# Optimization experiments

Hardware: AMD Instinct MI355X
Metric: run time of the kernel (lower is better)

Reference implementation:

```python
import jax, jax.numpy as jnp
import numpy as np

DIM = 256
HEADS = 8
HEAD_DIM = DIM // HEADS
SCALE = HEAD_DIM ** -0.5
SR = 2
EPS_MAP = 1e-6
EPS_LN = 1e-5


def token2map(x, loc, h, w):
    # x: [B,N,C] tokens, loc: [B,N,2] in [0,1] -> dense [B,h,w,C] via scatter-add mean.
    # kernel_size=1 in the original forward, so reconstruct_feature is a no-op.
    B, N, C = x.shape
    loc = jnp.clip(loc, 0.0, 1.0) * jnp.array([w - 1, h - 1], dtype=loc.dtype)
    loc = jnp.round(loc).astype(jnp.int32)
    idx = loc[..., 0] + loc[..., 1] * w + (jnp.arange(B, dtype=jnp.int32) * (h * w))[:, None]
    src = jnp.concatenate([x, jnp.ones((B, N, 1), x.dtype)], axis=-1).reshape(B * N, C + 1)
    out = jax.ops.segment_sum(src, idx.reshape(-1), num_segments=B * h * w)
    out = out.reshape(B, h, w, C + 1)
    feat, mask = out[..., :C], out[..., C:]
    feat = feat / (mask + EPS_MAP)
    mask = (mask > 0).astype(feat.dtype)
    return feat * mask  # [B,h,w,C]


def layernorm(x, g, b):
    mu = jnp.mean(x, axis=-1, keepdims=True)
    var = jnp.mean(jnp.square(x - mu), axis=-1, keepdims=True)
    return (x - mu) * jax.lax.rsqrt(var + EPS_LN) * g + b


def setup_inputs() -> dict:
    key = jax.random.key(0)
    ks = jax.random.split(key, 12)
    B, N, C = 4, 4096, DIM
    inp = {
        "x": jax.random.normal(ks[0], (B, N, C), jnp.float32),
        "x_source": jax.random.normal(ks[1], (B, N, C), jnp.float32),
        "loc_source": jax.random.uniform(ks[2], (B, N, 2), jnp.float32),
        "conf_source": jax.random.normal(ks[3], (B, N, 1), jnp.float32),
        "Wq": jax.random.normal(ks[4], (C, C), jnp.float32) * 0.02,
        "Wk": jax.random.normal(ks[5], (C, C), jnp.float32) * 0.02,
        "Wv": jax.random.normal(ks[6], (C, C), jnp.float32) * 0.02,
        "Wsr": jax.random.normal(ks[7], (C, C), jnp.float32) * 0.02,
        "b_sr": jnp.zeros((C,), jnp.float32),
        "ln_g": jnp.ones((C,), jnp.float32),
        "ln_b": jnp.zeros((C,), jnp.float32),
        "Wp": jax.random.normal(ks[8], (C, C), jnp.float32) * 0.02,
        "bp": jnp.zeros((C,), jnp.float32),
        "H": 64,
        "W": 64,
    }
    return inp


def reference(x, x_source, loc_source, conf_source, Wq, Wk, Wv, Wsr, b_sr, ln_g, ln_b, Wp, bp, H, W):
    B, N, C = x.shape
    h, w = H // SR, W // SR
    # queries
    q = (x @ Wq.T).reshape(B, N, HEADS, HEAD_DIM).transpose(0, 2, 1, 3)  # [B,h,N,d]
    # rasterize source tokens, 1x1 conv (sr) + LayerNorm
    xs = token2map(x_source, loc_source, h, w).reshape(B, h * w, C)
    xs = xs @ Wsr.T + b_sr
    xs = layernorm(xs, ln_g, ln_b)  # [B,Ns,C]
    Ns = h * w
    k = (xs @ Wk.T).reshape(B, Ns, HEADS, HEAD_DIM).transpose(0, 2, 1, 3)
    v = (xs @ Wv.T).reshape(B, Ns, HEADS, HEAD_DIM).transpose(0, 2, 1, 3)
    # rasterized confidence as additive bias
    conf = token2map(conf_source, loc_source, h, w).reshape(B, Ns)  # [B,Ns]
    attn = jnp.einsum("bhnd,bhmd->bhnm", q, k) * SCALE + conf[:, None, None, :]
    attn = jax.nn.softmax(attn, axis=-1)
    out = jnp.einsum("bhnm,bhmd->bhnd", attn, v).transpose(0, 2, 1, 3).reshape(B, N, C)
    return out @ Wp.T + bp
```

## Files before the change

### kernel.cpp

```cpp
#include <hip/hip_runtime.h>
#include <math.h>

#define DIMC   256
#define NQ     4096
#define BATCH  4
#define NS     1024
#define WG     32
#define HG     32
#define NHEADS 8
#define HDIM   32
#define TILEK  128
#define KSTRIDE 40
#define VSTRIDE 136
#define WSTRIDE 264
#define BUCKCAP 64
#define GCELLS 4
#define SCALE_ATTN 0.17677669529663687
#define LOG2E 1.4426950408889634
#define SCALE2F ((float)(SCALE_ATTN * LOG2E))

extern "C" __device__ float __ocml_native_exp2_f32(float);
#if __has_builtin(__builtin_amdgcn_exp2f)
#define EXP2(x) __builtin_amdgcn_exp2f(x)
#else
#define EXP2(x) __ocml_native_exp2_f32(x)
#endif

typedef _Float16 f16;
typedef __attribute__((ext_vector_type(8))) __bf16    bf16x8;
typedef __attribute__((ext_vector_type(8))) _Float16  f16x8;
typedef __attribute__((ext_vector_type(4))) _Float16  f16x4;
typedef __attribute__((ext_vector_type(4))) float     f32x4;

#define MFMA16B(A, B, C)  __builtin_amdgcn_mfma_f32_16x16x32_bf16((A), (B), (C), 0, 0, 0)
#define MFMA16F(A, B, C)  __builtin_amdgcn_mfma_f32_16x16x32_f16((A), (B), (C), 0, 0, 0)
#define MFMA16K16(A, B, C) __builtin_amdgcn_mfma_f32_16x16x16f16((A), (B), (C), 0, 0, 0)

static __device__ __forceinline__ unsigned short bf16_hi(float v) {
    return __builtin_bit_cast(unsigned short, (__bf16)v);
}

__global__ __launch_bounds__(256) void prep_kernel(
    const float* __restrict__ Wsr, const float* __restrict__ Wq,
    const float* __restrict__ Wk, const float* __restrict__ Wv,
    const float* __restrict__ Wp,
    unsigned short* __restrict__ wsrh, unsigned short* __restrict__ wsrl,
    f16* __restrict__ wq16, f16* __restrict__ wkv, f16* __restrict__ wp16,
    int* __restrict__ cursor)
{
    int m = blockIdx.y;
    if (m == 5) {
        int i = blockIdx.x * 256 + threadIdx.x;
        if (i < BATCH * NS) cursor[i] = 0;
        return;
    }
    int i = (blockIdx.x * 256 + threadIdx.x) * 4;
    if (m == 0) {
        float4 v = *(const float4*)(Wsr + i);
        float vv[4] = {v.x, v.y, v.z, v.w};
        ushort4 h, l;
        unsigned short* hp = &h.x; unsigned short* lp = &l.x;
        #pragma unroll
        for (int j = 0; j < 4; j++) {
            __bf16 hb = (__bf16)vv[j];
            hp[j] = __builtin_bit_cast(unsigned short, hb);
            lp[j] = bf16_hi(vv[j] - (float)hb);
        }
        *(ushort4*)(wsrh + i) = h;
        *(ushort4*)(wsrl + i) = l;
    } else {
        const float* W = (m == 1) ? Wq : (m == 2) ? Wk : (m == 3) ? Wv : Wp;
        f16* O = (m == 1) ? wq16 : (m == 2) ? wkv
               : (m == 3) ? (wkv + DIMC * DIMC) : wp16;
        float4 v = *(const float4*)(W + i);
        f16x4 h = {(f16)v.x, (f16)v.y, (f16)v.z, (f16)v.w};
        *(f16x4*)(O + i) = h;
    }
}

__global__ __launch_bounds__(256) void build_kernel(
    const float* __restrict__ loc, int* __restrict__ cursor,
    int* __restrict__ bucket)
{
    int token = blockIdx.x * 256 + threadIdx.x;
    int b = token >> 12;
    float lx = loc[token * 2 + 0];
    float ly = loc[token * 2 + 1];
    lx = fminf(fmaxf(lx, 0.f), 1.f) * (float)(WG - 1);
    ly = fminf(fmaxf(ly, 0.f), 1.f) * (float)(HG - 1);
    int ix = (int)rintf(lx);
    int iy = (int)rintf(ly);
    int cell = b * NS + iy * WG + ix;
    int slot = atomicAdd(&cursor[cell], 1);
    if (slot < BUCKCAP) bucket[cell * BUCKCAP + slot] = token;
}

__global__ __launch_bounds__(256) void gather_kernel(
    const float* __restrict__ xsrc, const float* __restrict__ csrc,
    const int* __restrict__ cursor, const int* __restrict__ bucket,
    float* __restrict__ feat, float* __restrict__ cnt, float* __restrict__ confsum)
{
    __shared__ int bks[GCELLS][BUCKCAP];
    __shared__ int ns[GCELLS];
    int cell0 = blockIdx.x * GCELLS;
    int tid = threadIdx.x;
    int jw = tid >> 6, slot = tid & 63;
    int cj = cell0 + jw;
    int rawn = cursor[cj];
    if (slot == 0) ns[jw] = min(rawn, BUCKCAP);
    bks[jw][slot] = bucket[(size_t)cj * BUCKCAP + slot];
    __syncthreads();
    int nw = ns[jw];
    float cv = (slot < nw) ? csrc[bks[jw][slot]] : 0.f;
    #pragma unroll
    for (int off = 1; off < 64; off <<= 1) cv += __shfl_xor(cv, off);
    if (slot == 0) { confsum[cj] = cv; cnt[cj] = (float)rawn; }
    int c = tid;
    for (int j = 0; j < GCELLS; j++) {
        int n = ns[j];
        float s0 = 0.f, s1 = 0.f, s2 = 0.f, s3 = 0.f;
        int i = 0;
        for (; i + 4 <= n; i += 4) {
            s0 += xsrc[(size_t)bks[j][i]     * DIMC + c];
            s1 += xsrc[(size_t)bks[j][i + 1] * DIMC + c];
            s2 += xsrc[(size_t)bks[j][i + 2] * DIMC + c];
            s3 += xsrc[(size_t)bks[j][i + 3] * DIMC + c];
        }
        for (; i < n; i++)
            s0 += xsrc[(size_t)bks[j][i] * DIMC + c];
        feat[(size_t)(cell0 + j) * DIMC + c] = (s0 + s1) + (s2 + s3);
    }
}

__global__ __launch_bounds__(256) void gemm_sr_kernel(
    const float* __restrict__ A, const float* __restrict__ cnt,
    const float* __restrict__ confsum,
    const unsigned short* __restrict__ Whi, const unsigned short* __restrict__ Wlo,
    const float* __restrict__ bias, float* __restrict__ outF,
    float2* __restrict__ stats, float* __restrict__ conf2)
{
    int r0 = blockIdx.x * 16;
    int wave = threadIdx.x >> 6;
    int lane = threadIdx.x & 63;
    int s = lane & 15, g = lane >> 4;
    int arow = r0 + s;
    int cb = wave * 64;
    const float* ap = A + (size_t)arow * DIMC + 8 * g;
    float cv = cnt[arow];
    float invr = (cv > 0.f) ? 1.f / (cv + 1e-6f) : 0.f;

    f32x4 acc[4];
    #pragma unroll
    for (int cf = 0; cf < 4; cf++) {
        float bv = bias[cb + cf * 16 + s];
        acc[cf] = (f32x4){bv, bv, bv, bv};
    }

    #pragma unroll
    for (int kk = 0; kk < 8; kk++) {
        float4 a0 = *(const float4*)(ap + kk * 32);
        float4 a1 = *(const float4*)(ap + kk * 32 + 4);
        float av[8] = {a0.x, a0.y, a0.z, a0.w, a1.x, a1.y, a1.z, a1.w};
        bf16x8 ah, al;
        #pragma unroll
        for (int j = 0; j < 8; j++) {
            float v = av[j] * invr;
            __bf16 hb = (__bf16)v;
            ah[j] = hb;
            al[j] = (__bf16)(v - (float)hb);
        }
        #pragma unroll
        for (int cf = 0; cf < 4; cf++) {
            size_t woff = (size_t)(cb + cf * 16 + s) * DIMC + kk * 32 + 8 * g;
            bf16x8 bh = *(const bf16x8*)(Whi + woff);
            bf16x8 bl = *(const bf16x8*)(Wlo + woff);
            acc[cf] = MFMA16B(ah, bh, acc[cf]);
            acc[cf] = MFMA16B(al, bh, acc[cf]);
            acc[cf] = MFMA16B(ah, bl, acc[cf]);
        }
    }

    int rbase = r0 + 4 * g;
    #pragma unroll
    for (int cf = 0; cf < 4; cf++) {
        int c = cb + cf * 16 + s;
        #pragma unroll
        for (int r = 0; r < 4; r++)
            outF[(size_t)(rbase + r) * DIMC + c] = acc[cf][r];
    }
    float psum[4], psq[4];
    #pragma unroll
    for (int r = 0; r < 4; r++) {
        psum[r] = 0.f; psq[r] = 0.f;
        #pragma unroll
        for (int cf = 0; cf < 4; cf++) {
            float v = acc[cf][r];
            psum[r] += v; psq[r] += v * v;
        }
    }
    #pragma unroll
    for (int off = 1; off < 16; off <<= 1)
        #pragma unroll
        for (int r = 0; r < 4; r++) {
            psum[r] += __shfl_xor(psum[r], off);
            psq[r]  += __shfl_xor(psq[r], off);
        }
    __shared__ float ssum[4][16], ssq[4][16];
    if (s == 0)
        #pragma unroll
        for (int r = 0; r < 4; r++) {
            ssum[wave][4 * g + r] = psum[r];
            ssq[wave][4 * g + r]  = psq[r];
        }
    __syncthreads();
    if (threadIdx.x < 16) {
        int rr = threadIdx.x;
        float su = ssum[0][rr] + ssum[1][rr] + ssum[2][rr] + ssum[3][rr];
        float sq = ssq[0][rr] + ssq[1][rr] + ssq[2][rr] + ssq[3][rr];
        float mu  = su * (1.f / DIMC);
        float var = sq * (1.f / DIMC) - mu * mu;
        stats[r0 + rr] = make_float2(mu, rsqrtf(var + 1e-5f));
        float cv2 = cnt[r0 + rr];
        float iv2 = (cv2 > 0.f) ? 1.f / (cv2 + 1e-6f) : 0.f;
        conf2[r0 + rr] = confsum[r0 + rr] * iv2 * (float)LOG2E;
    }
}

__global__ __launch_bounds__(256) void gemm_kv_kernel(
    const float* __restrict__ xs, const float2* __restrict__ stats,
    const float* __restrict__ lng, const float* __restrict__ lnb,
    const f16* __restrict__ wkv, f16* __restrict__ k16, f16* __restrict__ vt16)
{
    int r0 = blockIdx.x * 16;
    int cb0 = blockIdx.y * 128;
    int wave = threadIdx.x >> 6;
    int lane = threadIdx.x & 63;
    int s = lane & 15, g = lane >> 4;
    int arow = r0 + s;
    int cb = cb0 + wave * 32;
    float2 st = stats[arow];
    const float* ap = xs + (size_t)arow * DIMC + 8 * g;

    f32x4 acc[2];
    acc[0] = (f32x4){0.f, 0.f, 0.f, 0.f};
    acc[1] = (f32x4){0.f, 0.f, 0.f, 0.f};

    #pragma unroll
    for (int kk = 0; kk < 8; kk++) {
        float4 a0 = *(const float4*)(ap + kk * 32);
        float4 a1 = *(const float4*)(ap + kk * 32 + 4);
        float4 g0 = *(const float4*)(lng + kk * 32 + 8 * g);
        float4 g1 = *(const float4*)(lng + kk * 32 + 8 * g + 4);
        float4 b0 = *(const float4*)(lnb + kk * 32 + 8 * g);
        float4 b1 = *(const float4*)(lnb + kk * 32 + 8 * g + 4);
        float av[8] = {a0.x, a0.y, a0.z, a0.w, a1.x, a1.y, a1.z, a1.w};
        float gv[8] = {g0.x, g0.y, g0.z, g0.w, g1.x, g1.y, g1.z, g1.w};
        float bv[8] = {b0.x, b0.y, b0.z, b0.w, b1.x, b1.y, b1.z, b1.w};
        f16x8 a;
        #pragma unroll
        for (int j = 0; j < 8; j++)
            a[j] = (f16)(((av[j] - st.x) * st.y) * gv[j] + bv[j]);
        #pragma unroll
        for (int cf = 0; cf < 2; cf++) {
            f16x8 bfrag = *(const f16x8*)(wkv + (size_t)(cb + cf * 16 + s) * DIMC
                                              + kk * 32 + 8 * g);
            acc[cf] = MFMA16F(a, bfrag, acc[cf]);
        }
    }

    int rbase = r0 + 4 * g;
    if (cb0 < 256) {
        #pragma unroll
        for (int cf = 0; cf < 2; cf++) {
            int c = cb + cf * 16 + s;
            #pragma unroll
            for (int r = 0; r < 4; r++)
                k16[(size_t)(rbase + r) * DIMC + c] = (f16)acc[cf][r];
        }
    } else {
        int b = rbase >> 10;
        int key0 = rbase & 1023;
        #pragma unroll
        for (int cf = 0; cf < 2; cf++) {
            int cc = cb + cf * 16 + s - 256;
            f16x4 h;
            #pragma unroll
            for (int r = 0; r < 4; r++) h[r] = (f16)acc[cf][r];
            size_t off = ((size_t)(b * DIMC + cc)) * NS + key0;
            *(f16x4*)(vt16 + off) = h;
        }
    }
}

template <bool A16, bool OUT16, bool HASBIAS>
__global__ __launch_bounds__(256) void gemm_lds_kernel(
    const void* __restrict__ Ain, const f16* __restrict__ W,
    const float* __restrict__ bias, float* __restrict__ outF,
    f16* __restrict__ out16)
{
    __shared__ f16 Bs[64 * WSTRIDE];
    int r0 = blockIdx.x * 64;
    int c0 = blockIdx.y * 64;
    int tid = threadIdx.x;
    for (int i = tid; i < 64 * 32; i += 256) {
        int row = i >> 5, seg = i & 31;
        *(f16x8*)(&Bs[row * WSTRIDE + seg * 8]) =
            *(const f16x8*)(W + (size_t)(c0 + row) * DIMC + seg * 8);
    }
    __syncthreads();
    int wave = tid >> 6;
    int lane = tid & 63;
    int s = lane & 15, g = lane >> 4;
    int arow = r0 + wave * 16 + s;

    f32x4 acc[4];
    #pragma unroll
    for (int cf = 0; cf < 4; cf++) {
        float bv = HASBIAS ? bias[c0 + cf * 16 + s] : 0.f;
        acc[cf] = (f32x4){bv, bv, bv, bv};
    }

    #pragma unroll
    for (int kk = 0; kk < 8; kk++) {
        f16x8 a;
        if (A16) {
            a = *(const f16x8*)((const f16*)Ain + (size_t)arow * DIMC + kk * 32 + 8 * g);
        } else {
            const float* ap = (const float*)Ain + (size_t)arow * DIMC + kk * 32 + 8 * g;
            float4 a0 = *(const float4*)ap;
            float4 a1 = *(const float4*)(ap + 4);
            a = (f16x8){(f16)a0.x, (f16)a0.y, (f16)a0.z, (f16)a0.w,
                        (f16)a1.x, (f16)a1.y, (f16)a1.z, (f16)a1.w};
        }
        #pragma unroll
        for (int cf = 0; cf < 4; cf++) {
            f16x8 bfrag = *(const f16x8*)(&Bs[(cf * 16 + s) * WSTRIDE + kk * 32 + 8 * g]);
            acc[cf] = MFMA16F(a, bfrag, acc[cf]);
        }
    }

    int rbase = r0 + wave * 16 + 4 * g;
    #pragma unroll
    for (int cf = 0; cf < 4; cf++) {
        int c = c0 + cf * 16 + s;
        #pragma unroll
        for (int r = 0; r < 4; r++) {
            if (OUT16) out16[(size_t)(rbase + r) * DIMC + c] = (f16)acc[cf][r];
            else       outF [(size_t)(rbase + r) * DIMC + c] = acc[cf][r];
        }
    }
}

__global__ __launch_bounds__(512) void attn_mfma_kernel(
    const f16* __restrict__ qbuf, const f16* __restrict__ kbuf,
    const f16* __restrict__ vt16, const float* __restrict__ conf2,
    f16* __restrict__ abuf)
{
    __shared__ f16 Ks[2][TILEK * KSTRIDE];
    __shared__ f16 Vs[2][HDIM * VSTRIDE];

    int blk  = blockIdx.x;
    int qt   = blk & 15;
    int bh   = blk >> 4;
    int hh   = bh & (NHEADS - 1);
    int b    = bh >> 3;
    int wave = threadIdx.x >> 6;
    int lane = threadIdx.x & 63;
    int s = lane & 15, g = lane >> 4;
    int q0 = qt * 256 + wave * 32;
    int tid = threadIdx.x;

    int kr = tid >> 2, khc = tid & 3;
    int vr = tid >> 4, vjc = tid & 15;
    const f16* kgb = kbuf + ((size_t)(b * NS)) * DIMC + hh * HDIM;
    const f16* vgb = vt16 + ((size_t)(bh * HDIM)) * NS;

    f16x8 qh[2];
    #pragma unroll
    for (int qf = 0; qf < 2; qf++)
        qh[qf] = *(const f16x8*)(qbuf +
            ((size_t)(b * NQ + q0 + qf * 16 + s)) * DIMC + hh * HDIM + 8 * g);

    f32x4 oacc[2][2];
    #pragma unroll
    for (int qf = 0; qf < 2; qf++)
        #pragma unroll
        for (int m = 0; m < 2; m++)
            oacc[qf][m] = (f32x4){0.f, 0.f, 0.f, 0.f};
    float lpart[2] = {0.f, 0.f};

    const float* cfb = conf2 + b * NS + 4 * g;

    f16x8 kA, vA;
    kA = *(const f16x8*)(kgb + (size_t)kr * DIMC + khc * 8);
    vA = *(const f16x8*)(vgb + (size_t)vr * NS + vjc * 8);
    *(f16x8*)(&Ks[0][kr * KSTRIDE + khc * 8]) = kA;
    *(f16x8*)(&Vs[0][vr * VSTRIDE + vjc * 8]) = vA;
    __syncthreads();

    for (int t = 0; t < NS / TILEK; t++) {
        int cur = t & 1;
        if (t < NS / TILEK - 1) {
            int kt = (t + 1) * TILEK;
            kA = *(const f16x8*)(kgb + (size_t)(kt + kr) * DIMC + khc * 8);
            vA = *(const f16x8*)(vgb + (size_t)vr * NS + kt + vjc * 8);
        }
        #pragma unroll
        for (int kc = 0; kc < TILEK / 32; kc++) {
            int krow = kc * 32;
            int k0g  = t * TILEK + krow;
            f16x8 khf[2];
            #pragma unroll
            for (int f = 0; f < 2; f++)
                khf[f] = *(const f16x8*)(&Ks[cur][(krow + 16 * f + s) * KSTRIDE + 8 * g]);
            f16x4 vtf[2][2];
            #pragma unroll
            for (int f = 0; f < 2; f++)
                #pragma unroll
                for (int m = 0; m < 2; m++)
                    vtf[f][m] = *(const f16x4*)(&Vs[cur][(16 * m + s) * VSTRIDE
                                                         + krow + 16 * f + 4 * g]);
            float4 cq[2];
            #pragma unroll
            for (int f = 0; f < 2; f++)
                cq[f] = *(const float4*)(cfb + k0g + 16 * f);

            #pragma unroll
            for (int qf = 0; qf < 2; qf++) {
                f32x4 sa[2];
                #pragma unroll
                for (int f = 0; f < 2; f++) {
                    f32x4 z = (f32x4){0.f, 0.f, 0.f, 0.f};
                    sa[f] = MFMA16F(khf[f], qh[qf], z);
                }
                float p[2][4];
                #pragma unroll
                for (int f = 0; f < 2; f++) {
                    const float* cp = &cq[f].x;
                    #pragma unroll
                    for (int r = 0; r < 4; r++) {
                        p[f][r] = EXP2(sa[f][r] * SCALE2F + cp[r]);
                        lpart[qf] += p[f][r];
                    }
                }
                #pragma unroll
                for (int f = 0; f < 2; f++) {
                    union { unsigned u[2]; f16x4 v; } Bp;
                    Bp.u[0] = __builtin_bit_cast(unsigned,
                        __builtin_amdgcn_cvt_pkrtz(p[f][0], p[f][1]));
                    Bp.u[1] = __builtin_bit_cast(unsigned,
                        __builtin_amdgcn_cvt_pkrtz(p[f][2], p[f][3]));
                    #pragma unroll
                    for (int m = 0; m < 2; m++)
                        oacc[qf][m] = MFMA16K16(vtf[f][m], Bp.v, oacc[qf][m]);
                }
            }
        }
        if (t < NS / TILEK - 1) {
            int nxt = cur ^ 1;
            *(f16x8*)(&Ks[nxt][kr * KSTRIDE + khc * 8]) = kA;
            *(f16x8*)(&Vs[nxt][vr * VSTRIDE + vjc * 8]) = vA;
            __syncthreads();
        }
    }

    #pragma unroll
    for (int qf = 0; qf < 2; qf++) {
        float l = lpart[qf];
        l += __shfl_xor(l, 16);
        l += __shfl_xor(l, 32);
        float invl = 1.f / l;
        f16* orow = abuf + ((size_t)(b * NQ + q0 + qf * 16 + s)) * DIMC + hh * HDIM;
        #pragma unroll
        for (int m = 0; m < 2; m++) {
            f16x4 o;
            #pragma unroll
            for (int r = 0; r < 4; r++) o[r] = (f16)(oacc[qf][m][r] * invl);
            *(f16x4*)(orow + 16 * m + 4 * g) = o;
        }
    }
}

extern "C" void kernel_launch(void* const* d_in, const int* in_sizes, int n_in,
                              void* d_out, int out_size, void* d_ws, size_t ws_size,
                              hipStream_t stream)
{
    (void)in_sizes; (void)n_in; (void)out_size; (void)ws_size;
    const float* x    = (const float*)d_in[0];
    const float* xsrc = (const float*)d_in[1];
    const float* loc  = (const float*)d_in[2];
    const float* csrc = (const float*)d_in[3];
    const float* Wq   = (const float*)d_in[4];
    const float* Wk   = (const float*)d_in[5];
    const float* Wv   = (const float*)d_in[6];
    const float* Wsr  = (const float*)d_in[7];
    const float* bsr  = (const float*)d_in[8];
    const float* lng  = (const float*)d_in[9];
    const float* lnb  = (const float*)d_in[10];
    const float* Wp   = (const float*)d_in[11];
    const float* bp   = (const float*)d_in[12];

    const int MS = BATCH * NS * DIMC;
    const int MQ = BATCH * NQ * DIMC;
    const int WSZ = DIMC * DIMC;

    float* ws      = (float*)d_ws;
    float* feat    = ws;
    float* cnt     = feat + MS;
    float* confsum = cnt + BATCH * NS;
    float* xs      = confsum + BATCH * NS;
    float* conf2   = xs + MS;
    float2* stats  = (float2*)(conf2 + BATCH * NS);
    int* cursor    = (int*)(stats + BATCH * NS);
    int* bucket    = cursor + BATCH * NS;
    f16* q16    = (f16*)(bucket + BATCH * NS * BUCKCAP);
    f16* k16    = q16 + MQ;
    f16* vt16   = k16 + MS;
    f16* abuf16 = vt16 + MS;
    unsigned short* wsrh = (unsigned short*)(abuf16 + MQ);
    unsigned short* wsrl = wsrh + WSZ;
    f16* wq16 = (f16*)(wsrl + WSZ);
    f16* wkv  = wq16 + WSZ;
    f16* wp16 = wkv + 2 * WSZ;
    float* outp = (float*)d_out;

    prep_kernel<<<dim3(64, 6), 256, 0, stream>>>(
        Wsr, Wq, Wk, Wv, Wp, wsrh, wsrl, wq16, wkv, wp16, cursor);
    build_kernel<<<BATCH * NQ / 256, 256, 0, stream>>>(loc, cursor, bucket);
    gather_kernel<<<BATCH * NS / GCELLS, 256, 0, stream>>>(
        xsrc, csrc, cursor, bucket, feat, cnt, confsum);
    gemm_sr_kernel<<<BATCH * NS / 16, 256, 0, stream>>>(
        feat, cnt, confsum, wsrh, wsrl, bsr, xs, stats, conf2);
    gemm_lds_kernel<false, true, false><<<dim3(BATCH * NQ / 64, 4), 256, 0, stream>>>(
        x, wq16, nullptr, nullptr, q16);
    gemm_kv_kernel<<<dim3(BATCH * NS / 16, 4), 256, 0, stream>>>(
        xs, stats, lng, lnb, wkv, k16, vt16);
    attn_mfma_kernel<<<BATCH * NHEADS * (NQ / 256), 512, 0, stream>>>(
        q16, k16, vt16, conf2, abuf16);
    gemm_lds_kernel<true, false, true><<<dim3(BATCH * NQ / 64, 4), 256, 0, stream>>>(
        abuf16, wp16, bp, outp, nullptr);
}
```

Baseline: 106.8 us.

## Split attention over key halves and merge partials in the output projection

```diff
diff --git a/kernel.cpp b/kernel.cpp
--- a/kernel.cpp
+++ b/kernel.cpp
@@ -15,6 +15,7 @@
 #define WSTRIDE 264
 #define BUCKCAP 64
 #define GCELLS 4
+#define NSPLIT 2
 #define SCALE_ATTN 0.17677669529663687
 #define LOG2E 1.4426950408889634
 #define SCALE2F ((float)(SCALE_ATTN * LOG2E))
@@ -292,9 +293,10 @@
     }
 }
 
-template <bool A16, bool OUT16, bool HASBIAS>
+template <bool A16, bool OUT16, bool HASBIAS, bool COMBINE>
 __global__ __launch_bounds__(256) void gemm_lds_kernel(
-    const void* __restrict__ Ain, const f16* __restrict__ W,
+    const void* __restrict__ Ain, const f16* __restrict__ Ain2,
+    const float* __restrict__ lsum, const f16* __restrict__ W,
     const float* __restrict__ bias, float* __restrict__ outF,
     f16* __restrict__ out16)
 {
@@ -323,7 +325,17 @@
     #pragma unroll
     for (int kk = 0; kk < 8; kk++) {
         f16x8 a;
-        if (A16) {
+        if (COMBINE) {
+            f16x8 x0 = *(const f16x8*)((const f16*)Ain + (size_t)arow * DIMC + kk * 32 + 8 * g);
+            f16x8 x1 = *(const f16x8*)(Ain2 + (size_t)arow * DIMC + kk * 32 + 8 * g);
+            float l0 = lsum[(size_t)arow * NHEADS + kk];
+            float l1 = lsum[((size_t)(BATCH * NQ) + arow) * NHEADS + kk];
+            float w = 1.f / (l0 + l1);
+            float w0 = l0 * w, w1 = l1 * w;
+            #pragma unroll
+            for (int j = 0; j < 8; j++)
+                a[j] = (f16)(w0 * (float)x0[j] + w1 * (float)x1[j]);
+        } else if (A16) {
             a = *(const f16x8*)((const f16*)Ain + (size_t)arow * DIMC + kk * 32 + 8 * g);
         } else {
             const float* ap = (const float*)Ain + (size_t)arow * DIMC + kk * 32 + 8 * g;
@@ -354,14 +366,16 @@
 __global__ __launch_bounds__(512) void attn_mfma_kernel(
     const f16* __restrict__ qbuf, const f16* __restrict__ kbuf,
     const f16* __restrict__ vt16, const float* __restrict__ conf2,
-    f16* __restrict__ abuf)
+    f16* __restrict__ opart, float* __restrict__ lsum)
 {
     __shared__ f16 Ks[2][TILEK * KSTRIDE];
     __shared__ f16 Vs[2][HDIM * VSTRIDE];
 
     int blk  = blockIdx.x;
-    int qt   = blk & 15;
-    int bh   = blk >> 4;
+    int split = blk >> 9;
+    int rem  = blk & 511;
+    int qt   = rem & 15;
+    int bh   = rem >> 4;
     int hh   = bh & (NHEADS - 1);
     int b    = bh >> 3;
     int wave = threadIdx.x >> 6;
@@ -391,16 +405,20 @@
 
     const float* cfb = conf2 + b * NS + 4 * g;
 
+    int tstart = split * (NS / TILEK / NSPLIT);
+    int tend   = tstart + NS / TILEK / NSPLIT;
+    int kbase  = tstart * TILEK;
+
     f16x8 kA, vA;
-    kA = *(const f16x8*)(kgb + (size_t)kr * DIMC + khc * 8);
-    vA = *(const f16x8*)(vgb + (size_t)vr * NS + vjc * 8);
+    kA = *(const f16x8*)(kgb + (size_t)(kbase + kr) * DIMC + khc * 8);
+    vA = *(const f16x8*)(vgb + (size_t)vr * NS + kbase + vjc * 8);
     *(f16x8*)(&Ks[0][kr * KSTRIDE + khc * 8]) = kA;
     *(f16x8*)(&Vs[0][vr * VSTRIDE + vjc * 8]) = vA;
     __syncthreads();
 
-    for (int t = 0; t < NS / TILEK; t++) {
-        int cur = t & 1;
-        if (t < NS / TILEK - 1) {
+    for (int t = tstart; t < tend; t++) {
+        int cur = (t - tstart) & 1;
+        if (t < tend - 1) {
             int kt = (t + 1) * TILEK;
             kA = *(const f16x8*)(kgb + (size_t)(kt + kr) * DIMC + khc * 8);
             vA = *(const f16x8*)(vgb + (size_t)vr * NS + kt + vjc * 8);
@@ -456,7 +474,7 @@
                 }
             }
         }
-        if (t < NS / TILEK - 1) {
+        if (t < tend - 1) {
             int nxt = cur ^ 1;
             *(f16x8*)(&Ks[nxt][kr * KSTRIDE + khc * 8]) = kA;
             *(f16x8*)(&Vs[nxt][vr * VSTRIDE + vjc * 8]) = vA;
@@ -464,13 +482,15 @@
         }
     }
 
+    f16* obase = opart + (size_t)split * ((size_t)BATCH * NQ * DIMC);
     #pragma unroll
     for (int qf = 0; qf < 2; qf++) {
         float l = lpart[qf];
         l += __shfl_xor(l, 16);
         l += __shfl_xor(l, 32);
         float invl = 1.f / l;
-        f16* orow = abuf + ((size_t)(b * NQ + q0 + qf * 16 + s)) * DIMC + hh * HDIM;
+        int q = q0 + qf * 16 + s;
+        f16* orow = obase + ((size_t)(b * NQ + q)) * DIMC + hh * HDIM;
         #pragma unroll
         for (int m = 0; m < 2; m++) {
             f16x4 o;
@@ -478,6 +498,8 @@
             for (int r = 0; r < 4; r++) o[r] = (f16)(oacc[qf][m][r] * invl);
             *(f16x4*)(orow + 16 * m + 4 * g) = o;
         }
+        if (g == 0)
+            lsum[((size_t)split * (BATCH * NQ) + b * NQ + q) * NHEADS + hh] = l;
     }
 }
 
@@ -516,8 +538,9 @@
     f16* q16    = (f16*)(bucket + BATCH * NS * BUCKCAP);
     f16* k16    = q16 + MQ;
     f16* vt16   = k16 + MS;
-    f16* abuf16 = vt16 + MS;
-    unsigned short* wsrh = (unsigned short*)(abuf16 + MQ);
+    f16* opart  = vt16 + MS;
+    float* lsum = (float*)(opart + (size_t)NSPLIT * MQ);
+    unsigned short* wsrh = (unsigned short*)(lsum + (size_t)NSPLIT * BATCH * NQ * NHEADS);
     unsigned short* wsrl = wsrh + WSZ;
     f16* wq16 = (f16*)(wsrl + WSZ);
     f16* wkv  = wq16 + WSZ;
@@ -531,12 +554,12 @@
         xsrc, csrc, cursor, bucket, feat, cnt, confsum);
     gemm_sr_kernel<<<BATCH * NS / 16, 256, 0, stream>>>(
         feat, cnt, confsum, wsrh, wsrl, bsr, xs, stats, conf2);
-    gemm_lds_kernel<false, true, false><<<dim3(BATCH * NQ / 64, 4), 256, 0, stream>>>(
-        x, wq16, nullptr, nullptr, q16);
+    gemm_lds_kernel<false, true, false, false><<<dim3(BATCH * NQ / 64, 4), 256, 0, stream>>>(
+        x, nullptr, nullptr, wq16, nullptr, nullptr, q16);
     gemm_kv_kernel<<<dim3(BATCH * NS / 16, 4), 256, 0, stream>>>(
         xs, stats, lng, lnb, wkv, k16, vt16);
-    attn_mfma_kernel<<<BATCH * NHEADS * (NQ / 256), 512, 0, stream>>>(
-        q16, k16, vt16, conf2, abuf16);
-    gemm_lds_kernel<true, false, true><<<dim3(BATCH * NQ / 64, 4), 256, 0, stream>>>(
-        abuf16, wp16, bp, outp, nullptr);
-}
+    attn_mfma_kernel<<<NSPLIT * BATCH * NHEADS * (NQ / 256), 512, 0, stream>>>(
+        q16, k16, vt16, conf2, opart, lsum);
+    gemm_lds_kernel<true, false, true, true><<<dim3(BATCH * NQ / 64, 4), 256, 0, stream>>>(
+        opart, opart + (size_t)MQ, lsum, wp16, bp, outp, nullptr);
+}
```

Result: slower. 112.1 us (+4.9%).
